# Optimization experiments

Measured on AMD Instinct MI355X. Metric: run time of the kernel, lower is better.

The kernel has to match this reference:

```python
import jax, jax.numpy as jnp
import numpy as np

EPS = 1e-5

def setup_inputs() -> dict:
    key = jax.random.key(0)
    k1, k2, k3, k4, k5 = jax.random.split(key, 5)
    N, E, D = 50000, 1600000, 128
    feat = jax.random.normal(k1, (N, D), dtype=jnp.float32)
    edge_index = jax.random.randint(k2, (2, E), 0, N, dtype=jnp.int64)
    W = jax.random.normal(k3, (D, D), dtype=jnp.float32) * (1.0 / np.sqrt(D))
    b = jax.random.normal(k4, (D,), dtype=jnp.float32) * 0.01
    gamma = jnp.ones((D,), dtype=jnp.float32)
    beta = jnp.zeros((D,), dtype=jnp.float32)
    return {"feat": feat, "edge_index": edge_index, "W": W, "b": b, "gamma": gamma, "beta": beta}

def reference(feat, edge_index, W, b, gamma, beta):
    # feat: [N, D] node features; edge_index: [2, E] (src, dst)
    N = feat.shape[0]
    src, dst = edge_index[0], edge_index[1]
    ones = jnp.ones(src.shape, dtype=feat.dtype)
    # out-degree of source nodes, in-degree of destination nodes
    deg_out = jnp.clip(jax.ops.segment_sum(ones, src, num_segments=N), 1.0)
    deg_in = jnp.clip(jax.ops.segment_sum(ones, dst, num_segments=N), 1.0)
    # pre-scale by D_out^{-1/2}, aggregate messages (copy_src + sum)
    feat_src = feat * jax.lax.rsqrt(deg_out)[:, None]        # [N, D]
    agg = jax.ops.segment_sum(feat_src[src], dst, num_segments=N)  # [N, D]
    # linear projection then post-scale by D_in^{-1/2}
    rst = agg @ W.T + b
    rst = rst * jax.lax.rsqrt(deg_in)[:, None]
    # identity residual (in_dim == out_dim)
    rst = rst + feat
    # LayerNorm(out_dim)
    mu = jnp.mean(rst, axis=-1, keepdims=True)
    var = jnp.var(rst, axis=-1, keepdims=True)
    rst = (rst - mu) * jax.lax.rsqrt(var + EPS) * gamma + beta
    # relu activation
    return jax.nn.relu(rst)
```

## Files before the change

### kernel.cpp

```cpp
#include <hip/hip_runtime.h>
#include <hip/hip_fp16.h>

#define LN_EPS 1e-5f
#define D 128
#define TN 16
#define NT 8
#define BCAP 768
#define MAXB 4096
#define BBLK 128
#define HBLK 2048

__global__ __launch_bounds__(256) void k_build(const int* __restrict__ ei, int E,
        int* __restrict__ cnt_out, int* __restrict__ bcnt,
        unsigned int* __restrict__ bkt, int NB) {
    __shared__ int h[MAXB];
    __shared__ int cur[MAXB];
    int tid = threadIdx.x;
    int E4 = E >> 2;
    const int4* src4 = (const int4*)ei;
    const int4* dst4 = (const int4*)(ei + E);

    if (blockIdx.x >= BBLK) {
        int gtid = (blockIdx.x - BBLK) * 256 + tid;
        int gstride = (gridDim.x - BBLK) * 256;
        for (int i = gtid; i < E4; i += gstride) {
            int4 s = src4[i];
            atomicAdd(&cnt_out[s.x], 1);
            atomicAdd(&cnt_out[s.y], 1);
            atomicAdd(&cnt_out[s.z], 1);
            atomicAdd(&cnt_out[s.w], 1);
        }
        for (int e = (E4 << 2) + gtid; e < E; e += gstride) {
            atomicAdd(&cnt_out[ei[e]], 1);
        }
        return;
    }

    int chunk4 = (E4 + BBLK - 1) / BBLK;
    int lo4 = blockIdx.x * chunk4;
    int hi4 = min(E4, lo4 + chunk4);
    bool last = (blockIdx.x == BBLK - 1);

    for (int k = tid; k < NB; k += 256) h[k] = 0;
    __syncthreads();

    for (int i = lo4 + tid; i < hi4; i += 256) {
        int4 d = dst4[i];
        atomicAdd(&h[d.x >> 4], 1);
        atomicAdd(&h[d.y >> 4], 1);
        atomicAdd(&h[d.z >> 4], 1);
        atomicAdd(&h[d.w >> 4], 1);
    }
    if (last) {
        for (int e = (E4 << 2) + tid; e < E; e += 256)
            atomicAdd(&h[ei[E + e] >> 4], 1);
    }
    __syncthreads();

    for (int k = tid; k < NB; k += 256) {
        int c = h[k];
        cur[k] = c ? atomicAdd(&bcnt[k], c) : 0;
    }
    __syncthreads();

    for (int i = lo4 + tid; i < hi4; i += 256) {
        int4 s = src4[i];
        int4 d = dst4[i];
        int p0 = atomicAdd(&cur[d.x >> 4], 1);
        int p1 = atomicAdd(&cur[d.y >> 4], 1);
        int p2 = atomicAdd(&cur[d.z >> 4], 1);
        int p3 = atomicAdd(&cur[d.w >> 4], 1);
        if (p0 < BCAP) bkt[(size_t)(d.x >> 4) * BCAP + p0] = (unsigned)s.x | ((unsigned)(d.x & 15) << 16);
        if (p1 < BCAP) bkt[(size_t)(d.y >> 4) * BCAP + p1] = (unsigned)s.y | ((unsigned)(d.y & 15) << 16);
        if (p2 < BCAP) bkt[(size_t)(d.z >> 4) * BCAP + p2] = (unsigned)s.z | ((unsigned)(d.z & 15) << 16);
        if (p3 < BCAP) bkt[(size_t)(d.w >> 4) * BCAP + p3] = (unsigned)s.w | ((unsigned)(d.w & 15) << 16);
    }
    if (last) {
        for (int e = (E4 << 2) + tid; e < E; e += 256) {
            int s = ei[e], dd = ei[E + e];
            int p = atomicAdd(&cur[dd >> 4], 1);
            if (p < BCAP) bkt[(size_t)(dd >> 4) * BCAP + p] = (unsigned)s | ((unsigned)(dd & 15) << 16);
        }
    }
}

__global__ __launch_bounds__(256) void k_rs(const int* __restrict__ cnt_out,
                                            float* __restrict__ rs_out,
                                            const float* __restrict__ W,
                                            float* __restrict__ Wt, int N) {
    int i = blockIdx.x * blockDim.x + threadIdx.x;
    if (i < N) rs_out[i] = rsqrtf((float)max(cnt_out[i], 1));
    if (i < D * D) {
        int r = i >> 7, c = i & 127;
        Wt[c * D + r] = W[i];
    }
}

__global__ __launch_bounds__(256) void k_prep(const float4* __restrict__ feat4,
                                              const float* __restrict__ rs_out,
                                              ushort4* __restrict__ feat_h,
                                              int total ) {
    int stride = gridDim.x * blockDim.x;
    for (int i = blockIdx.x * blockDim.x + threadIdx.x; i < total; i += stride) {
        int n = i >> 5;
        float rs = rs_out[n];
        float4 f = feat4[i];
        __half2 lo = __floats2half2_rn(f.x * rs, f.y * rs);
        __half2 hi = __floats2half2_rn(f.z * rs, f.w * rs);
        ushort4 u;
        u.x = __half_as_ushort(__low2half(lo));
        u.y = __half_as_ushort(__high2half(lo));
        u.z = __half_as_ushort(__low2half(hi));
        u.w = __half_as_ushort(__high2half(hi));
        feat_h[i] = u;
    }
}

__global__ __launch_bounds__(256) void k_fused(
        const int* __restrict__ bcnt, const unsigned int* __restrict__ bkt,
        const __half2* __restrict__ feat_h, const float* __restrict__ Wt,
        const float* __restrict__ bias, const float* __restrict__ gamma,
        const float* __restrict__ beta, const float* __restrict__ feat,
        float* __restrict__ out, int N) {
    __shared__ float aggT[TN][D];
    __shared__ float redS[2][2][NT];
    __shared__ float redQ[2][2][NT];
    __shared__ unsigned int braw[BCAP];
    __shared__ unsigned short blist[BCAP];
    __shared__ int bstart[TN + 1];
    __shared__ int bfill[TN];
    __shared__ int bdeg[TN];

    int tid  = threadIdx.x;
    int wv   = tid >> 6;
    int lane = tid & 63;
    int g    = tid >> 7;
    int d    = tid & 127;
    int w2   = (tid >> 6) & 1;

    float bd  = bias[d];
    float gd  = gamma[d];
    float btd = beta[d];

    int ntiles = (N + TN - 1) / TN;
    for (int t = blockIdx.x; t < ntiles; t += gridDim.x) {
        int nbase = t * TN;
        __syncthreads();

        if (tid < TN) { bdeg[tid] = 0; bfill[tid] = 0; }
        __syncthreads();
        int ecnt = min(bcnt[t], BCAP);
        for (int j = tid; j < ecnt; j += 256) {
            unsigned int v = bkt[(size_t)t * BCAP + j];
            braw[j] = v;
            atomicAdd(&bdeg[v >> 16], 1);
        }
        __syncthreads();
        if (tid == 0) {
            int run = 0;
            #pragma unroll
            for (int i = 0; i < TN; ++i) { bstart[i] = run; run += bdeg[i]; }
            bstart[TN] = run;
        }
        __syncthreads();
        for (int j = tid; j < ecnt; j += 256) {
            unsigned int v = braw[j];
            int node = v >> 16;
            int slot = bstart[node] + atomicAdd(&bfill[node], 1);
            blist[slot] = (unsigned short)(v & 0xFFFF);
        }
        __syncthreads();

        for (int i = 0; i < 4; ++i) {
            int li = wv * 4 + i;
            int n  = nbase + li;
            float2 acc = make_float2(0.0f, 0.0f);
            if (n < N) {
                int deg = bdeg[li];
                int st  = bstart[li];
                int m8  = deg & ~7;
                int j   = 0;
                for (; j < m8; j += 8) {
                    int ss[8];
                    #pragma unroll
                    for (int k = 0; k < 8; ++k) ss[k] = blist[st + j + k];
                    __half2 hh[8];
                    #pragma unroll
                    for (int k = 0; k < 8; ++k)
                        hh[k] = feat_h[(size_t)ss[k] * 64 + lane];
                    #pragma unroll
                    for (int k = 0; k < 8; ++k) {
                        float2 f = __half22float2(hh[k]);
                        acc.x += f.x; acc.y += f.y;
                    }
                }
                for (; j < deg; ++j) {
                    int s = blist[st + j];
                    float2 f = __half22float2(feat_h[(size_t)s * 64 + lane]);
                    acc.x += f.x; acc.y += f.y;
                }
            }
            ((float2*)aggT[li])[lane] = acc;
        }
        __syncthreads();

        float acc[NT];
        #pragma unroll
        for (int j = 0; j < NT; ++j) acc[j] = 0.0f;

        #pragma unroll 4
        for (int k = 0; k < D; ++k) {
            float w = Wt[(size_t)k * D + d];
            #pragma unroll
            for (int j = 0; j < NT; ++j)
                acc[j] = fmaf(aggT[g * NT + j][k], w, acc[j]);
        }

        float r[NT], s[NT], q[NT];
        #pragma unroll
        for (int j = 0; j < NT; ++j) {
            int li = g * NT + j;
            int n  = nbase + li;
            float ri = 0.0f;
            if (n < N) {
                float rsin = rsqrtf((float)max(bdeg[li], 1));
                ri = (acc[j] + bd) * rsin + feat[(size_t)n * D + d];
            }
            r[j] = ri;
            s[j] = ri;
            q[j] = ri * ri;
        }

        #pragma unroll
        for (int j = 0; j < NT; ++j) {
            for (int off = 32; off > 0; off >>= 1) {
                s[j] += __shfl_down(s[j], off);
                q[j] += __shfl_down(q[j], off);
            }
        }
        if (lane == 0) {
            #pragma unroll
            for (int j = 0; j < NT; ++j) { redS[g][w2][j] = s[j]; redQ[g][w2][j] = q[j]; }
        }
        __syncthreads();

        #pragma unroll
        for (int j = 0; j < NT; ++j) {
            int n = nbase + g * NT + j;
            if (n < N) {
                float S  = redS[g][0][j] + redS[g][1][j];
                float Q  = redQ[g][0][j] + redQ[g][1][j];
                float mu = S * (1.0f / 128.0f);
                float var = Q * (1.0f / 128.0f) - mu * mu;
                float v = (r[j] - mu) * rsqrtf(var + LN_EPS) * gd + btd;
                out[(size_t)n * D + d] = fmaxf(v, 0.0f);
            }
        }
    }
}

extern "C" void kernel_launch(void* const* d_in, const int* in_sizes, int n_in,
                              void* d_out, int out_size, void* d_ws, size_t ws_size,
                              hipStream_t stream) {
    const float* feat  = (const float*)d_in[0];
    const int*   ei    = (const int*)  d_in[1];
    const float* W     = (const float*)d_in[2];
    const float* bias  = (const float*)d_in[3];
    const float* gamma = (const float*)d_in[4];
    const float* beta  = (const float*)d_in[5];
    float* out = (float*)d_out;

    const int N  = in_sizes[0] / D;
    const int E  = in_sizes[1] / 2;
    const int NB = (N + TN - 1) / TN;

    const size_t Np  = ((size_t)N + 1023) & ~(size_t)1023;
    const size_t NBp = ((size_t)NB + 1023) & ~(size_t)1023;
    int*   cnt_out = (int*)d_ws;
    int*   bcnt    = cnt_out + Np;
    float* rs_out  = (float*)(bcnt + NBp);
    float* Wt      = rs_out + Np;
    unsigned int* bkt = (unsigned int*)(Wt + D * D);
    ushort4* feat_h   = (ushort4*)(bkt + (size_t)NB * BCAP);

    hipMemsetAsync(d_ws, 0, (Np + NBp) * sizeof(int), stream);

    k_build<<<BBLK + HBLK, 256, 0, stream>>>(ei, E, cnt_out, bcnt, bkt, NB);
    int nblk = (max(N, D * D) + 255) / 256;
    k_rs<<<nblk, 256, 0, stream>>>(cnt_out, rs_out, W, Wt, N);
    k_prep<<<2048, 256, 0, stream>>>((const float4*)feat, rs_out, feat_h, N * 32);
    k_fused<<<NB, 256, 0, stream>>>(bcnt, bkt,
                                    (const __half2*)feat_h, Wt, bias, gamma,
                                    beta, feat, out, N);
}
```

Before: 218.0 us.

## Replace scalar FP32 GEMM in fused kernel with FP16 MFMA and register-held weights

The per-tile 16x128x128 projection now runs on MFMA 16x16x16 f16 instructions instead of scalar FMAs over fp32 weights read from global memory. W is converted to half once, and each wave keeps its two 16-column weight slices in registers for the whole persistent loop. The aggregated features are stored in shared memory as fp16 with a padded stride, and the LayerNorm reduction is rewritten to match the MFMA output layout. This removes repeated global weight loads and scalar FMA work, but rounding aggregates and weights to fp16 lowers precision.

```diff
diff --git a/kernel.cpp b/kernel.cpp
--- a/kernel.cpp
+++ b/kernel.cpp
@@ -4,11 +4,14 @@
 #define LN_EPS 1e-5f
 #define D 128
 #define TN 16
-#define NT 8
 #define BCAP 768
 #define MAXB 4096
 #define BBLK 128
 #define HBLK 2048
+#define AGG_LD 136
+
+typedef _Float16 f16x4 __attribute__((ext_vector_type(4)));
+typedef float f32x4 __attribute__((ext_vector_type(4)));
 
 __global__ __launch_bounds__(256) void k_build(const int* __restrict__ ei, int E,
         int* __restrict__ cnt_out, int* __restrict__ bcnt,
@@ -87,12 +90,12 @@
 __global__ __launch_bounds__(256) void k_rs(const int* __restrict__ cnt_out,
                                             float* __restrict__ rs_out,
                                             const float* __restrict__ W,
-                                            float* __restrict__ Wt, int N) {
+                                            __half2* __restrict__ Wh2, int N) {
     int i = blockIdx.x * blockDim.x + threadIdx.x;
     if (i < N) rs_out[i] = rsqrtf((float)max(cnt_out[i], 1));
-    if (i < D * D) {
-        int r = i >> 7, c = i & 127;
-        Wt[c * D + r] = W[i];
+    if (i < D * D / 2) {
+        float2 w2 = ((const float2*)W)[i];
+        Wh2[i] = __floats2half2_rn(w2.x, w2.y);
     }
 }
 
@@ -118,13 +121,13 @@
 
 __global__ __launch_bounds__(256) void k_fused(
         const int* __restrict__ bcnt, const unsigned int* __restrict__ bkt,
-        const __half2* __restrict__ feat_h, const float* __restrict__ Wt,
+        const __half2* __restrict__ feat_h, const _Float16* __restrict__ Wh,
         const float* __restrict__ bias, const float* __restrict__ gamma,
         const float* __restrict__ beta, const float* __restrict__ feat,
         float* __restrict__ out, int N) {
-    __shared__ float aggT[TN][D];
-    __shared__ float redS[2][2][NT];
-    __shared__ float redQ[2][2][NT];
+    __shared__ _Float16 aggH[TN * AGG_LD];
+    __shared__ float redS[4][TN];
+    __shared__ float redQ[4][TN];
     __shared__ unsigned int braw[BCAP];
     __shared__ unsigned short blist[BCAP];
     __shared__ int bstart[TN + 1];
@@ -134,13 +137,21 @@
     int tid  = threadIdx.x;
     int wv   = tid >> 6;
     int lane = tid & 63;
-    int g    = tid >> 7;
-    int d    = tid & 127;
-    int w2   = (tid >> 6) & 1;
-
-    float bd  = bias[d];
-    float gd  = gamma[d];
-    float btd = beta[d];
+    int l15  = lane & 15;
+    int lg   = lane >> 4;
+
+    int dA0 = (wv * 2 + 0) * 16 + l15;
+    int dA1 = (wv * 2 + 1) * 16 + l15;
+    float bd0 = bias[dA0],  bd1 = bias[dA1];
+    float gd0 = gamma[dA0], gd1 = gamma[dA1];
+    float bt0 = beta[dA0],  bt1 = beta[dA1];
+
+    f16x4 Bf0[8], Bf1[8];
+    #pragma unroll
+    for (int kb = 0; kb < 8; ++kb) {
+        Bf0[kb] = *reinterpret_cast<const f16x4*>(&Wh[(size_t)dA0 * D + kb * 16 + lg * 4]);
+        Bf1[kb] = *reinterpret_cast<const f16x4*>(&Wh[(size_t)dA1 * D + kb * 16 + lg * 4]);
+    }
 
     int ntiles = (N + TN - 1) / TN;
     for (int t = blockIdx.x; t < ntiles; t += gridDim.x) {
@@ -200,60 +211,56 @@
                     acc.x += f.x; acc.y += f.y;
                 }
             }
-            ((float2*)aggT[li])[lane] = acc;
-        }
-        __syncthreads();
-
-        float acc[NT];
+            *reinterpret_cast<__half2*>(&aggH[li * AGG_LD + 2 * lane]) =
+                __floats2half2_rn(acc.x, acc.y);
+        }
+        __syncthreads();
+
+        f32x4 acc0 = {0.0f, 0.0f, 0.0f, 0.0f};
+        f32x4 acc1 = {0.0f, 0.0f, 0.0f, 0.0f};
         #pragma unroll
-        for (int j = 0; j < NT; ++j) acc[j] = 0.0f;
-
-        #pragma unroll 4
-        for (int k = 0; k < D; ++k) {
-            float w = Wt[(size_t)k * D + d];
-            #pragma unroll
-            for (int j = 0; j < NT; ++j)
-                acc[j] = fmaf(aggT[g * NT + j][k], w, acc[j]);
-        }
-
-        float r[NT], s[NT], q[NT];
+        for (int kb = 0; kb < 8; ++kb) {
+            f16x4 a = *reinterpret_cast<const f16x4*>(&aggH[l15 * AGG_LD + kb * 16 + lg * 4]);
+            acc0 = __builtin_amdgcn_mfma_f32_16x16x16f16(a, Bf0[kb], acc0, 0, 0, 0);
+            acc1 = __builtin_amdgcn_mfma_f32_16x16x16f16(a, Bf1[kb], acc1, 0, 0, 0);
+        }
+
+        float rv0[4], rv1[4];
         #pragma unroll
-        for (int j = 0; j < NT; ++j) {
-            int li = g * NT + j;
-            int n  = nbase + li;
-            float ri = 0.0f;
+        for (int r = 0; r < 4; ++r) {
+            int m = lg * 4 + r;
+            int n = nbase + m;
+            float f0 = 0.0f, f1 = 0.0f;
             if (n < N) {
-                float rsin = rsqrtf((float)max(bdeg[li], 1));
-                ri = (acc[j] + bd) * rsin + feat[(size_t)n * D + d];
+                float rsin = rsqrtf((float)max(bdeg[m], 1));
+                f0 = (acc0[r] + bd0) * rsin + feat[(size_t)n * D + dA0];
+                f1 = (acc1[r] + bd1) * rsin + feat[(size_t)n * D + dA1];
             }
-            r[j] = ri;
-            s[j] = ri;
-            q[j] = ri * ri;
-        }
+            rv0[r] = f0; rv1[r] = f1;
+            float s = f0 + f1;
+            float q = f0 * f0 + f1 * f1;
+            s += __shfl_xor(s, 1);  q += __shfl_xor(q, 1);
+            s += __shfl_xor(s, 2);  q += __shfl_xor(q, 2);
+            s += __shfl_xor(s, 4);  q += __shfl_xor(q, 4);
+            s += __shfl_xor(s, 8);  q += __shfl_xor(q, 8);
+            if (l15 == 0) { redS[wv][m] = s; redQ[wv][m] = q; }
+        }
+        __syncthreads();
 
         #pragma unroll
-        for (int j = 0; j < NT; ++j) {
-            for (int off = 32; off > 0; off >>= 1) {
-                s[j] += __shfl_down(s[j], off);
-                q[j] += __shfl_down(q[j], off);
-            }
-        }
-        if (lane == 0) {
-            #pragma unroll
-            for (int j = 0; j < NT; ++j) { redS[g][w2][j] = s[j]; redQ[g][w2][j] = q[j]; }
-        }
-        __syncthreads();
-
-        #pragma unroll
-        for (int j = 0; j < NT; ++j) {
-            int n = nbase + g * NT + j;
+        for (int r = 0; r < 4; ++r) {
+            int m = lg * 4 + r;
+            int n = nbase + m;
             if (n < N) {
-                float S  = redS[g][0][j] + redS[g][1][j];
-                float Q  = redQ[g][0][j] + redQ[g][1][j];
-                float mu = S * (1.0f / 128.0f);
+                float S = redS[0][m] + redS[1][m] + redS[2][m] + redS[3][m];
+                float Q = redQ[0][m] + redQ[1][m] + redQ[2][m] + redQ[3][m];
+                float mu  = S * (1.0f / 128.0f);
                 float var = Q * (1.0f / 128.0f) - mu * mu;
-                float v = (r[j] - mu) * rsqrtf(var + LN_EPS) * gd + btd;
-                out[(size_t)n * D + d] = fmaxf(v, 0.0f);
+                float inv = rsqrtf(var + LN_EPS);
+                float v0 = (rv0[r] - mu) * inv * gd0 + bt0;
+                float v1 = (rv1[r] - mu) * inv * gd1 + bt1;
+                out[(size_t)n * D + dA0] = fmaxf(v0, 0.0f);
+                out[(size_t)n * D + dA1] = fmaxf(v1, 0.0f);
             }
         }
     }
@@ -279,17 +286,17 @@
     int*   cnt_out = (int*)d_ws;
     int*   bcnt    = cnt_out + Np;
     float* rs_out  = (float*)(bcnt + NBp);
-    float* Wt      = rs_out + Np;
-    unsigned int* bkt = (unsigned int*)(Wt + D * D);
+    _Float16* Wh   = (_Float16*)(rs_out + Np);
+    unsigned int* bkt = (unsigned int*)((int*)(rs_out + Np) + D * D / 2);
     ushort4* feat_h   = (ushort4*)(bkt + (size_t)NB * BCAP);
 
     hipMemsetAsync(d_ws, 0, (Np + NBp) * sizeof(int), stream);
 
     k_build<<<BBLK + HBLK, 256, 0, stream>>>(ei, E, cnt_out, bcnt, bkt, NB);
-    int nblk = (max(N, D * D) + 255) / 256;
-    k_rs<<<nblk, 256, 0, stream>>>(cnt_out, rs_out, W, Wt, N);
+    int nblk = (max(N, D * D / 2) + 255) / 256;
+    k_rs<<<nblk, 256, 0, stream>>>(cnt_out, rs_out, W, (__half2*)Wh, N);
     k_prep<<<2048, 256, 0, stream>>>((const float4*)feat, rs_out, feat_h, N * 32);
     k_fused<<<NB, 256, 0, stream>>>(bcnt, bkt,
-                                    (const __half2*)feat_h, Wt, bias, gamma,
+                                    (const __half2*)feat_h, Wh, bias, gamma,
                                     beta, feat, out, N);
 }
```

New measurement: 208.6 us. -4.3%, faster.
